# Kernel optimization log

Hardware: AMD Instinct MI355X
Metric: run time of the kernel (lower is better)

## Reference

```python
import jax, jax.numpy as jnp
import numpy as np

HEADS = 8
DIM_HEAD = 64
TOP_K = 1024
KMEANS_ITERS = 4  # the original KMeans class is external; we use Lloyd's algorithm, init = first TOP_K points


def chan_ln(x, g, b):
    # ChanLayerNorm3D: normalize over channel dim (axis=1), biased variance
    m = x.mean(axis=1, keepdims=True)
    v = x.var(axis=1, keepdims=True)
    return g.reshape(1, -1, 1, 1, 1) * (x - m) / (jnp.sqrt(v) + 1e-6) + b.reshape(1, -1, 1, 1, 1)


def kmeans_fit(x, k, iters):
    # x: [N, d] -> centroids [k, d]
    cent0 = x[:k]

    def step(_, cent):
        d2 = (x * x).sum(-1, keepdims=True) - 2.0 * (x @ cent.T) + (cent * cent).sum(-1)
        assign = jnp.argmin(d2, axis=-1)
        sums = jax.ops.segment_sum(x, assign, num_segments=k)
        cnt = jax.ops.segment_sum(jnp.ones((x.shape[0],), x.dtype), assign, num_segments=k)
        new = sums / jnp.maximum(cnt, 1.0)[:, None]
        return jnp.where(cnt[:, None] > 0, new, cent)  # keep old centroid for empty clusters

    return jax.lax.fori_loop(0, iters, step, cent0)


def select_best_idx(q, k, top_k):
    # q: [B, i, d], k: [B, j, d] -> indices [B, top_k] of keys farthest (L1) from their assigned q-centroid
    B, j, d = k.shape
    qf = q.reshape(-1, d)
    kf = k.reshape(-1, d)
    cent = kmeans_fit(qf, top_k, KMEANS_ITERS)
    d2 = (kf * kf).sum(-1, keepdims=True) - 2.0 * (kf @ cent.T) + (cent * cent).sum(-1)
    kc = jnp.argmin(d2, axis=-1)  # predict cluster of each key
    centers = cent[kc].reshape(B, j, d)
    dist = jnp.abs(centers - k).sum(-1)  # [B, j], L1 distance to assigned centroid
    return jnp.argsort(-dist, axis=1)[:, :top_k]


def dpca(query_source, context, w_q, w_kv, w_out, cn_g, cn_b, qn_g, qn_b, on_g, on_b, gamma):
    b, c, D, H, W = query_source.shape
    ctx = chan_ln(context, cn_g, cn_b)
    qs = chan_ln(query_source, qn_g, qn_b)
    # 1x1x1 convs == per-voxel channel matmuls
    kv = jnp.einsum('oc,bcdhw->bodhw', w_kv, ctx)
    k3, v3 = jnp.split(kv, 2, axis=1)
    q3 = jnp.einsum('oc,bcdhw->bodhw', w_q, qs)

    def fold_flat(t, norm):
        bb = t.shape[0]
        t = t.reshape(bb * HEADS, DIM_HEAD, *t.shape[2:])  # fold heads into batch
        if norm:  # F.normalize over channel dim, eps=1e-12
            t = t / jnp.maximum(jnp.linalg.norm(t, axis=1, keepdims=True), 1e-12)
        return t.reshape(bb * HEADS, DIM_HEAD, -1).transpose(0, 2, 1)  # [B, tokens, d]

    q = fold_flat(q3, True)
    k = fold_flat(k3, True)
    v = fold_flat(v3, False)

    idx = select_best_idx(jax.lax.stop_gradient(q), jax.lax.stop_gradient(k), TOP_K)
    k = jnp.take_along_axis(k, idx[:, :, None], axis=1)
    v = jnp.take_along_axis(v, idx[:, :, None], axis=1)

    attn = jax.nn.softmax(jnp.einsum('bid,bjd->bij', q, k), axis=-1)
    out = jnp.einsum('bij,bjd->bid', attn, v)
    out = out.reshape(b, HEADS, D, H, W, DIM_HEAD).transpose(0, 1, 5, 2, 3, 4)
    out = out.reshape(b, HEADS * DIM_HEAD, D, H, W)
    out = jnp.einsum('oc,bcdhw->bodhw', w_out, out)
    out = chan_ln(out, on_g, on_b)
    return gamma * out + query_source


def setup_inputs() -> dict:
    key = jax.random.key(0)
    ks = jax.random.split(key, 6)
    dim, inner, b = 256, HEADS * DIM_HEAD, 2
    query_source = jax.random.normal(ks[0], (b, dim, 16, 16, 16), jnp.float32)
    context = jax.random.normal(ks[1], (b, dim, 8, 16, 16), jnp.float32)
    s_in = 1.0 / np.sqrt(dim)
    return {
        'query_source': query_source,
        'context': context,
        'w_q': jax.random.normal(ks[2], (inner, dim), jnp.float32) * s_in,
        'w_kv': jax.random.normal(ks[3], (2 * inner, dim), jnp.float32) * s_in,
        'w_out': jax.random.normal(ks[4], (dim, inner), jnp.float32) * (1.0 / np.sqrt(inner)),
        'cn_g': jnp.ones((dim,), jnp.float32), 'cn_b': jnp.zeros((dim,), jnp.float32),
        'qn_g': jnp.ones((dim,), jnp.float32), 'qn_b': jnp.zeros((dim,), jnp.float32),
        'on_g': jnp.ones((dim,), jnp.float32), 'on_b': jnp.zeros((dim,), jnp.float32),
        'gamma': jnp.full((1,), 0.5, jnp.float32),  # torch inits to 0 (trivial output); 0.5 makes the test meaningful
    }


def reference(query_source, context, w_q, w_kv, w_out, cn_g, cn_b, qn_g, qn_b, on_g, on_b, gamma):
    return dpca(query_source, context, w_q, w_kv, w_out, cn_g, cn_b, qn_g, qn_b, on_g, on_b, gamma)
```

## Files before the change

### kernel.cpp

```cpp
#include <hip/hip_runtime.h>
#include <math.h>

#define BB 2
#define CDIM 256
#define NQ 4096
#define NK 2048
#define BH 16
#define TOPK 1024
#define NPQ (BH*NQ)
#define NPK (BH*NK)

typedef __attribute__((ext_vector_type(8))) short bfx8;
typedef __attribute__((ext_vector_type(8))) _Float16 hfx8;
typedef __attribute__((ext_vector_type(2))) __fp16 fpx2;
typedef __attribute__((ext_vector_type(4))) float fx4;
typedef __attribute__((ext_vector_type(4))) unsigned short us4;

__device__ inline unsigned short f2bf(float x) {
  unsigned u = __float_as_uint(x);
  return (unsigned short)((u + 0x7fffu + ((u >> 16) & 1u)) >> 16);
}
__device__ inline unsigned short f2h_bits(float x) {
  _Float16 h = (_Float16)x;
  unsigned short u;
  __builtin_memcpy(&u, &h, 2);
  return u;
}
__device__ inline float h_bits2f(unsigned short u) {
  _Float16 h;
  __builtin_memcpy(&h, &u, 2);
  return (float)h;
}

__global__ __launch_bounds__(256) void chan_ln_tsplit_k(
    const float* __restrict__ x, const float* __restrict__ g,
    const float* __restrict__ bta, unsigned short* __restrict__ yh,
    unsigned short* __restrict__ yl, int C, int N) {
  __shared__ float tile[4][64][65];
  __shared__ float p1[4][64], p2[4][64];
  __shared__ float mArr[64], invArr[64];
  int t = threadIdx.x, lane = t & 63, wv = t >> 6;
  int n0 = blockIdx.x * 64, bi = blockIdx.y;
  const float* xb = x + (size_t)bi * C * N + n0 + lane;
  float s = 0.f, s2 = 0.f;
  for (int cl = 0; cl < 64; ++cl) {
    float v = xb[(size_t)(wv * 64 + cl) * N];
    tile[wv][cl][lane] = v;
    s += v;
    s2 += v * v;
  }
  p1[wv][lane] = s;
  p2[wv][lane] = s2;
  __syncthreads();
  if (t < 64) {
    float ts = p1[0][t] + p1[1][t] + p1[2][t] + p1[3][t];
    float ts2 = p2[0][t] + p2[1][t] + p2[2][t] + p2[3][t];
    float m = ts / C;
    float var = ts2 / C - m * m;
    mArr[t] = m;
    invArr[t] = 1.f / (sqrtf(fmaxf(var, 0.f)) + 1e-6f);
  }
  __syncthreads();
  int c = wv * 64 + lane;
  float gc = g[c], bc = bta[c];
  unsigned short* ohb = yh + ((size_t)bi * N + n0) * C + c;
  unsigned short* olb = yl + ((size_t)bi * N + n0) * C + c;
  for (int pl = 0; pl < 64; ++pl) {
    float v = tile[wv][lane][pl];
    float ln = gc * (v - mArr[pl]) * invArr[pl] + bc;
    unsigned short hb = f2h_bits(ln);
    ohb[(size_t)pl * C] = hb;
    olb[(size_t)pl * C] = f2h_bits((ln - h_bits2f(hb)) * 2048.f);
  }
}

__global__ __launch_bounds__(256) void gemm_mfma_k(
    const float* __restrict__ W, const unsigned short* __restrict__ Xh,
    const unsigned short* __restrict__ Xl, float* __restrict__ Y,
    int O, int C, int N) {
  __shared__ __align__(16) unsigned short xlds[2][64][64];
  int t = threadIdx.x, lane = t & 63, wv = t >> 6;
  int lq = lane & 15, lg = lane >> 4;
  int n0 = blockIdx.x * 64, o0 = blockIdx.y * 64 + wv * 16;
  int b = blockIdx.z;
  const unsigned short* xbh = Xh + ((size_t)b * N + n0) * C;
  const unsigned short* xbl = Xl + ((size_t)b * N + n0) * C;
  const float* wr = W + (size_t)(o0 + lq) * C;

  int a = t * 16;
  int srow = a >> 6;
  int schunk = (a >> 4) & 3;
  const unsigned short* gsh = xbh + (size_t)srow * C + schunk * 8;
  const unsigned short* gsl = xbl + (size_t)srow * C + schunk * 8;
  int swz = (srow & 7) << 4;
  int wbh = srow * 128 + ((schunk * 16) ^ swz);
  int wbl = srow * 128 + ((64 + schunk * 16) ^ swz);
  int rswz = (lq & 7) << 4;
  int xh0 = (lg * 16) ^ rswz;
  int xl0 = (64 + lg * 16) ^ rswz;

  fx4 ahi[4], alo[4];
  for (int nt = 0; nt < 4; ++nt) {
    ahi[nt] = (fx4){0.f, 0.f, 0.f, 0.f};
    alo[nt] = (fx4){0.f, 0.f, 0.f, 0.f};
  }

  {
    uint4 h0 = *(const uint4*)(gsh);
    uint4 l0 = *(const uint4*)(gsl);
    *(uint4*)((char*)&xlds[0][0][0] + wbh) = h0;
    *(uint4*)((char*)&xlds[0][0][0] + wbl) = l0;
  }
  float4 w0c = *(const float4*)(wr + lg * 8);
  float4 w1c = *(const float4*)(wr + lg * 8 + 4);

  int nsteps = C / 32;
  for (int s = 0; s < nsteps; ++s) {
    int cur = s & 1;
    __syncthreads();
    uint4 nh, nl;
    float4 nw0, nw1;
    if (s < nsteps - 1) {
      nh = *(const uint4*)(gsh + (s + 1) * 32);
      nl = *(const uint4*)(gsl + (s + 1) * 32);
      nw0 = *(const float4*)(wr + (s + 1) * 32 + lg * 8);
      nw1 = *(const float4*)(wr + (s + 1) * 32 + lg * 8 + 4);
    }
    __builtin_amdgcn_sched_barrier(0);
    float wv8[8] = {w0c.x, w0c.y, w0c.z, w0c.w, w1c.x, w1c.y, w1c.z, w1c.w};
    hfx8 ah, al;
#pragma unroll
    for (int i = 0; i < 8; ++i) {
      _Float16 hh = (_Float16)wv8[i];
      ah[i] = hh;
      al[i] = (_Float16)((wv8[i] - (float)hh) * 2048.f);
    }
    const char* Xb = (const char*)&xlds[cur][0][0];
#pragma unroll
    for (int nt = 0; nt < 4; ++nt) {
      int rb = (nt * 16 + lq) * 128;
      hfx8 bh = *(const hfx8*)(Xb + rb + xh0);
      hfx8 bl = *(const hfx8*)(Xb + rb + xl0);
      ahi[nt] = __builtin_amdgcn_mfma_f32_16x16x32_f16(ah, bh, ahi[nt], 0, 0, 0);
      alo[nt] = __builtin_amdgcn_mfma_f32_16x16x32_f16(al, bh, alo[nt], 0, 0, 0);
      alo[nt] = __builtin_amdgcn_mfma_f32_16x16x32_f16(ah, bl, alo[nt], 0, 0, 0);
    }
    __builtin_amdgcn_sched_barrier(0);
    if (s < nsteps - 1) {
      *(uint4*)((char*)&xlds[cur ^ 1][0][0] + wbh) = nh;
      *(uint4*)((char*)&xlds[cur ^ 1][0][0] + wbl) = nl;
      w0c = nw0;
      w1c = nw1;
    }
  }
  float* yb = Y + ((size_t)b * O + o0) * N + n0;
#pragma unroll
  for (int nt = 0; nt < 4; ++nt)
#pragma unroll
    for (int r = 0; r < 4; ++r)
      yb[(size_t)(lg * 4 + r) * N + nt * 16 + lq] = ahi[nt][r] + alo[nt][r] * (1.f / 2048.f);
}

template <int PATH>
__global__ __launch_bounds__(256) void gemmfold_k(
    const float* __restrict__ W, const unsigned short* __restrict__ Xh,
    const unsigned short* __restrict__ Xl, float* __restrict__ fq,
    unsigned short* __restrict__ sh, unsigned short* __restrict__ sl,
    unsigned short* __restrict__ b16, float* __restrict__ fv,
    int C, int N) {
  __shared__ __align__(16) unsigned short xlds[2][64][64];
  __shared__ float ftile[64][65];
  __shared__ float part[4][64];
  __shared__ float invArr[64];
  int t = threadIdx.x, lane = t & 63, wv = t >> 6;
  int lq = lane & 15, lg = lane >> 4;
  int n0 = blockIdx.x * 64, o0 = blockIdx.y * 64 + wv * 16;
  int b = blockIdx.z;
  bool isV = (PATH == 1) && (blockIdx.y >= 8);
  int h = (PATH == 1) ? (blockIdx.y & 7) : blockIdx.y;
  const unsigned short* xbh = Xh + ((size_t)b * N + n0) * C;
  const unsigned short* xbl = Xl + ((size_t)b * N + n0) * C;
  const float* wr = W + (size_t)(o0 + lq) * C;

  int a = t * 16;
  int srow = a >> 6;
  int schunk = (a >> 4) & 3;
  const unsigned short* gsh = xbh + (size_t)srow * C + schunk * 8;
  const unsigned short* gsl = xbl + (size_t)srow * C + schunk * 8;
  int swz = (srow & 7) << 4;
  int wbh = srow * 128 + ((schunk * 16) ^ swz);
  int wbl = srow * 128 + ((64 + schunk * 16) ^ swz);
  int rswz = (lq & 7) << 4;
  int xh0 = (lg * 16) ^ rswz;
  int xl0 = (64 + lg * 16) ^ rswz;

  fx4 ahi[4], alo[4];
  for (int nt = 0; nt < 4; ++nt) {
    ahi[nt] = (fx4){0.f, 0.f, 0.f, 0.f};
    alo[nt] = (fx4){0.f, 0.f, 0.f, 0.f};
  }

  {
    uint4 h0 = *(const uint4*)(gsh);
    uint4 l0 = *(const uint4*)(gsl);
    *(uint4*)((char*)&xlds[0][0][0] + wbh) = h0;
    *(uint4*)((char*)&xlds[0][0][0] + wbl) = l0;
  }
  float4 w0c = *(const float4*)(wr + lg * 8);
  float4 w1c = *(const float4*)(wr + lg * 8 + 4);

  for (int s = 0; s < 8; ++s) {
    int cur = s & 1;
    __syncthreads();
    uint4 nh, nl;
    float4 nw0, nw1;
    if (s < 7) {
      nh = *(const uint4*)(gsh + (s + 1) * 32);
      nl = *(const uint4*)(gsl + (s + 1) * 32);
      nw0 = *(const float4*)(wr + (s + 1) * 32 + lg * 8);
      nw1 = *(const float4*)(wr + (s + 1) * 32 + lg * 8 + 4);
    }
    __builtin_amdgcn_sched_barrier(0);
    float wv8[8] = {w0c.x, w0c.y, w0c.z, w0c.w, w1c.x, w1c.y, w1c.z, w1c.w};
    hfx8 ah, al;
#pragma unroll
    for (int i = 0; i < 8; ++i) {
      _Float16 hh = (_Float16)wv8[i];
      ah[i] = hh;
      al[i] = (_Float16)((wv8[i] - (float)hh) * 2048.f);
    }
    const char* Xb = (const char*)&xlds[cur][0][0];
#pragma unroll
    for (int nt = 0; nt < 4; ++nt) {
      int rb = (nt * 16 + lq) * 128;
      hfx8 bh = *(const hfx8*)(Xb + rb + xh0);
      hfx8 bl = *(const hfx8*)(Xb + rb + xl0);
      ahi[nt] = __builtin_amdgcn_mfma_f32_16x16x32_f16(ah, bh, ahi[nt], 0, 0, 0);
      alo[nt] = __builtin_amdgcn_mfma_f32_16x16x32_f16(al, bh, alo[nt], 0, 0, 0);
      alo[nt] = __builtin_amdgcn_mfma_f32_16x16x32_f16(ah, bl, alo[nt], 0, 0, 0);
    }
    __builtin_amdgcn_sched_barrier(0);
    if (s < 7) {
      *(uint4*)((char*)&xlds[cur ^ 1][0][0] + wbh) = nh;
      *(uint4*)((char*)&xlds[cur ^ 1][0][0] + wbl) = nl;
      w0c = nw0;
      w1c = nw1;
    }
  }

  float val[4][4];
#pragma unroll
  for (int nt = 0; nt < 4; ++nt)
#pragma unroll
    for (int r = 0; r < 4; ++r)
      val[nt][r] = ahi[nt][r] + alo[nt][r] * (1.f / 2048.f);
  __syncthreads();
  if (!isV) {
#pragma unroll
    for (int nt = 0; nt < 4; ++nt) {
      float ss = val[nt][0] * val[nt][0] + val[nt][1] * val[nt][1] +
                 val[nt][2] * val[nt][2] + val[nt][3] * val[nt][3];
      ss += __shfl_xor(ss, 16);
      ss += __shfl_xor(ss, 32);
      if (lg == 0) part[wv][nt * 16 + lq] = ss;
    }
    __syncthreads();
    if (t < 64) {
      float tot = part[0][t] + part[1][t] + part[2][t] + part[3][t];
      invArr[t] = 1.f / fmaxf(sqrtf(tot), 1e-12f);
    }
    __syncthreads();
#pragma unroll
    for (int nt = 0; nt < 4; ++nt) {
      float iv = invArr[nt * 16 + lq];
#pragma unroll
      for (int r = 0; r < 4; ++r) val[nt][r] *= iv;
    }
    __syncthreads();
  }
#pragma unroll
  for (int nt = 0; nt < 4; ++nt)
#pragma unroll
    for (int r = 0; r < 4; ++r)
      ftile[nt * 16 + lq][wv * 16 + lg * 4 + r] = val[nt][r];
  __syncthreads();
  size_t rowb = (size_t)(b * 8 + h) * N + n0;
  for (int r2 = 0; r2 < 16; ++r2) {
    int n = r2 * 4 + wv;
    float v = ftile[n][lane];
    size_t idx = (rowb + n) * 64 + lane;
    if (PATH == 1 && isV) {
      fv[idx] = v;
    } else {
      fq[idx] = v;
      unsigned short hb = f2h_bits(v);
      sh[idx] = hb;
      sl[idx] = f2h_bits((v - h_bits2f(hb)) * 2048.f);
      if (PATH == 0) b16[idx] = hb;
    }
  }
}

__global__ void centprep_k(const float* __restrict__ cent, float* __restrict__ csq,
                           unsigned short* __restrict__ cb2h, unsigned short* __restrict__ cb2l) {
  int j = blockIdx.x, lane = threadIdx.x;
  float c = cent[j * 64 + lane];
  float s = c * c;
  for (int off = 32; off; off >>= 1) s += __shfl_xor(s, off);
  if (lane == 0) csq[j] = s;
  float m2 = -2.f * c;
  unsigned short h = f2h_bits(m2);
  cb2h[j * 64 + lane] = h;
  cb2l[j * 64 + lane] = f2h_bits((m2 - h_bits2f(h)) * 2048.f);
}

template <int DUO>
__global__ __launch_bounds__(256) void assign_mfma_k(
    const unsigned short* __restrict__ xh, const unsigned short* __restrict__ xl,
    const unsigned short* __restrict__ cb2h, const unsigned short* __restrict__ cb2l,
    const float* __restrict__ csq, int* __restrict__ aout) {
  __shared__ __align__(16) unsigned short clds[4][2][1024];
  int t = threadIdx.x, lane = t & 63, wv = t >> 6;
  int lq = lane & 15, lg = lane >> 4;
  int p0 = blockIdx.x * (DUO ? 128 : 64) + wv * (DUO ? 32 : 16);
  const unsigned short* xbA = xh + (size_t)(p0 + lq) * 64;
  const unsigned short* xlA = xl + (size_t)(p0 + lq) * 64;
  hfx8 ba0 = *(const hfx8*)(xbA + lg * 8);
  hfx8 ba1 = *(const hfx8*)(xbA + 32 + lg * 8);
  hfx8 la0 = *(const hfx8*)(xlA + lg * 8);
  hfx8 la1 = *(const hfx8*)(xlA + 32 + lg * 8);
  hfx8 bb0, bb1, lb0, lb1;
  if (DUO) {
    const unsigned short* xbB = xh + (size_t)(p0 + 16 + lq) * 64;
    const unsigned short* xlB = xl + (size_t)(p0 + 16 + lq) * 64;
    bb0 = *(const hfx8*)(xbB + lg * 8);
    bb1 = *(const hfx8*)(xbB + 32 + lg * 8);
    lb0 = *(const hfx8*)(xlB + lg * 8);
    lb1 = *(const hfx8*)(xlB + 32 + lg * 8);
  }

  int part = t >> 7;
  int abyte = (t & 127) * 16;
  int wbyte = abyte ^ (((abyte >> 7) & 7) << 4);
  const unsigned short* gsrc = (part ? cb2l : cb2h) + (abyte >> 1);
  int rowoff = lq * 128;
  int x0 = (lg * 16) ^ ((lq & 7) << 4);
  int x1 = (64 + lg * 16) ^ ((lq & 7) << 4);

  float bestA = 3.4e38f, bestB = 3.4e38f;
  int jA = 0, jB = 0;

  fx4 pchi0A, pclo0A, pchi1A, pclo1A;
  fx4 pchi0B, pclo0B, pchi1B, pclo1B;

  {
    uint4 r0 = *(const uint4*)(gsrc);
    uint4 r1 = *(const uint4*)(gsrc + 1024);
    *(uint4*)((char*)&clds[0][part][0] + wbyte) = r0;
    *(uint4*)((char*)&clds[1][part][0] + wbyte) = r1;
  }

#define COMPARE_PREV(SBASE)                                                    \
  {                                                                            \
    _Pragma("unroll")                                                          \
    for (int u = 0; u < 2; ++u) {                                              \
      int st_ = (SBASE) + u;                                                   \
      fx4 chi_ = u ? pchi1A : pchi0A;                                          \
      fx4 clo_ = u ? pclo1A : pclo0A;                                          \
      _Pragma("unroll")                                                        \
      for (int r_ = 0; r_ < 4; ++r_) {                                         \
        int j_ = st_ * 16 + lg * 4 + r_;                                       \
        float d2_ = chi_[r_] + clo_[r_] * (1.f / 2048.f);                      \
        if (d2_ < bestA) { bestA = d2_; jA = j_; }                             \
      }                                                                        \
      if (DUO) {                                                               \
        fx4 chiB_ = u ? pchi1B : pchi0B;                                       \
        fx4 cloB_ = u ? pclo1B : pclo0B;                                       \
        _Pragma("unroll")                                                      \
        for (int r_ = 0; r_ < 4; ++r_) {                                       \
          int j_ = st_ * 16 + lg * 4 + r_;                                     \
          float d2_ = chiB_[r_] + cloB_[r_] * (1.f / 2048.f);                  \
          if (d2_ < bestB) { bestB = d2_; jB = j_; }                           \
        }                                                                      \
      }                                                                        \
    }                                                                          \
  }

  for (int s = 0; s < 64; s += 2) {
    __syncthreads();
    uint4 rn0, rn1;
    if (s < 62) {
      rn0 = *(const uint4*)(gsrc + (size_t)(s + 2) * 1024);
      rn1 = *(const uint4*)(gsrc + (size_t)(s + 3) * 1024);
    }
    __builtin_amdgcn_sched_barrier(0);
    fx4 cchi0A, cclo0A, cchi1A, cclo1A;
    fx4 cchi0B, cclo0B, cchi1B, cclo1B;
#pragma unroll
    for (int u = 0; u < 2; ++u) {
      int st = s + u;
      const char* ph = (const char*)&clds[st & 3][0][0];
      const char* pl = (const char*)&clds[st & 3][1][0];
      hfx8 ah0 = *(const hfx8*)(ph + rowoff + x0);
      hfx8 ah1 = *(const hfx8*)(ph + rowoff + x1);
      hfx8 al0 = *(const hfx8*)(pl + rowoff + x0);
      hfx8 al1 = *(const hfx8*)(pl + rowoff + x1);
      fx4 cq = *(const fx4*)(csq + st * 16 + lg * 4);
      {
        fx4 chi = cq;
        chi = __builtin_amdgcn_mfma_f32_16x16x32_f16(ah0, ba0, chi, 0, 0, 0);
        chi = __builtin_amdgcn_mfma_f32_16x16x32_f16(ah1, ba1, chi, 0, 0, 0);
        fx4 clo = (fx4){0.f, 0.f, 0.f, 0.f};
        clo = __builtin_amdgcn_mfma_f32_16x16x32_f16(ah0, la0, clo, 0, 0, 0);
        clo = __builtin_amdgcn_mfma_f32_16x16x32_f16(ah1, la1, clo, 0, 0, 0);
        clo = __builtin_amdgcn_mfma_f32_16x16x32_f16(al0, ba0, clo, 0, 0, 0);
        clo = __builtin_amdgcn_mfma_f32_16x16x32_f16(al1, ba1, clo, 0, 0, 0);
        if (u == 0) { cchi0A = chi; cclo0A = clo; } else { cchi1A = chi; cclo1A = clo; }
      }
      if (DUO) {
        fx4 chi = cq;
        chi = __builtin_amdgcn_mfma_f32_16x16x32_f16(ah0, bb0, chi, 0, 0, 0);
        chi = __builtin_amdgcn_mfma_f32_16x16x32_f16(ah1, bb1, chi, 0, 0, 0);
        fx4 clo = (fx4){0.f, 0.f, 0.f, 0.f};
        clo = __builtin_amdgcn_mfma_f32_16x16x32_f16(ah0, lb0, clo, 0, 0, 0);
        clo = __builtin_amdgcn_mfma_f32_16x16x32_f16(ah1, lb1, clo, 0, 0, 0);
        clo = __builtin_amdgcn_mfma_f32_16x16x32_f16(al0, lb0 * (_Float16)0 + bb0, clo, 0, 0, 0);
        clo = __builtin_amdgcn_mfma_f32_16x16x32_f16(al1, bb1, clo, 0, 0, 0);
        if (u == 0) { cchi0B = chi; cclo0B = clo; } else { cchi1B = chi; cclo1B = clo; }
      }
    }
    if (s > 0) COMPARE_PREV(s - 2);
    pchi0A = cchi0A; pclo0A = cclo0A; pchi1A = cchi1A; pclo1A = cclo1A;
    if (DUO) { pchi0B = cchi0B; pclo0B = cclo0B; pchi1B = cchi1B; pclo1B = cclo1B; }
    __builtin_amdgcn_sched_barrier(0);
    if (s < 62) {
      *(uint4*)((char*)&clds[(s + 2) & 3][part][0] + wbyte) = rn0;
      *(uint4*)((char*)&clds[(s + 3) & 3][part][0] + wbyte) = rn1;
    }
  }
  COMPARE_PREV(62);
#undef COMPARE_PREV

  {
    float o = __shfl_xor(bestA, 16);
    int oj = __shfl_xor(jA, 16);
    if (o < bestA || (o == bestA && oj < jA)) { bestA = o; jA = oj; }
    o = __shfl_xor(bestA, 32);
    oj = __shfl_xor(jA, 32);
    if (o < bestA || (o == bestA && oj < jA)) { bestA = o; jA = oj; }
  }
  if (DUO) {
    float o = __shfl_xor(bestB, 16);
    int oj = __shfl_xor(jB, 16);
    if (o < bestB || (o == bestB && oj < jB)) { bestB = o; jB = oj; }
    o = __shfl_xor(bestB, 32);
    oj = __shfl_xor(jB, 32);
    if (o < bestB || (o == bestB && oj < jB)) { bestB = o; jB = oj; }
  }
  if (lg == 0) {
    aout[p0 + lq] = jA;
    if (DUO) aout[p0 + 16 + lq] = jB;
  }
}

__global__ void dist_k(const float* __restrict__ x, const float* __restrict__ cent,
                       const int* __restrict__ asg, float* __restrict__ dout) {
  int t = threadIdx.x, lane = t & 63, wv = t >> 6;
  int p = blockIdx.x * 4 + wv;
  int a = asg[p];
  float v = fabsf(cent[(size_t)a * 64 + lane] - x[(size_t)p * 64 + lane]);
  for (int off = 32; off; off >>= 1) v += __shfl_xor(v, off);
  if (lane == 0) dout[p] = v;
}

__global__ void segsum_k(const float* __restrict__ x, const int* __restrict__ asg,
                         float* __restrict__ sums, float* __restrict__ cnt) {
  int t = threadIdx.x, lane = t & 63, wv = t >> 6;
  int p = blockIdx.x * 4 + wv;
  int a = asg[p];
  float v = x[(size_t)p * 64 + lane];
  atomicAdd(&sums[a * 64 + lane], v);
  if (lane == 0) atomicAdd(&cnt[a], 1.0f);
}

__global__ __launch_bounds__(256) void centup_prep_k(
    float* __restrict__ cent, float* __restrict__ sums, float* __restrict__ cnt,
    float* __restrict__ csq, unsigned short* __restrict__ cb2h,
    unsigned short* __restrict__ cb2l) {
  int i = blockIdx.x * 256 + threadIdx.x;
  int j = i >> 6, lane = threadIdx.x & 63;
  float c = cnt[j];
  float oldc = cent[i];
  float newc = (c > 0.f) ? sums[i] / fmaxf(c, 1.f) : oldc;
  cent[i] = newc;
  float s = newc * newc;
  for (int off = 32; off; off >>= 1) s += __shfl_xor(s, off);
  if (lane == 0) csq[j] = s;
  float m2 = -2.f * newc;
  unsigned short h = f2h_bits(m2);
  cb2h[i] = h;
  cb2l[i] = f2h_bits((m2 - h_bits2f(h)) * 2048.f);
  sums[i] = 0.f;
  if (lane == 0) cnt[j] = 0.f;
}

__global__ __launch_bounds__(1024) void topk_k(const float* __restrict__ dist,
                                               int* __restrict__ sel) {
  __shared__ unsigned long long keys[2048];
  int bh = blockIdx.x, t = threadIdx.x;
  for (int i = t; i < 2048; i += 1024) {
    float d = dist[bh * 2048 + i];
    unsigned int db = __float_as_uint(d);
    keys[i] = ((unsigned long long)db << 32) | (unsigned int)(2047 - i);
  }
  __syncthreads();
  for (int k = 2; k <= 2048; k <<= 1) {
    for (int j = k >> 1; j > 0; j >>= 1) {
      for (int i = t; i < 2048; i += 1024) {
        int ixj = i ^ j;
        if (ixj > i) {
          unsigned long long a = keys[i], b = keys[ixj];
          bool up = ((i & k) == 0);
          bool sw = up ? (a < b) : (a > b);
          if (sw) { keys[i] = b; keys[ixj] = a; }
        }
      }
      __syncthreads();
    }
  }
  if (t < 1024) sel[bh * 1024 + t] = 2047 - (int)(keys[t] & 0xffffffffu);
}

__global__ void gatherb_k(const float* __restrict__ kbuf, const float* __restrict__ vbuf,
                          const int* __restrict__ sel, unsigned short* __restrict__ kh,
                          unsigned short* __restrict__ vT) {
  __shared__ unsigned short tile[64][66];
  int t = threadIdx.x, lane = t & 63, wv = t >> 6;
  int bh = blockIdx.y, i0 = blockIdx.x * 64;
  for (int r = 0; r < 16; ++r) {
    int i = r * 4 + wv;
    int src = sel[bh * 1024 + i0 + i];
    float kvv = kbuf[((size_t)bh * 2048 + src) * 64 + lane];
    kh[((size_t)bh * 1024 + i0 + i) * 64 + lane] = f2h_bits(kvv);
    float vv = vbuf[((size_t)bh * 2048 + src) * 64 + lane];
    tile[i][lane] = f2h_bits(vv);
  }
  __syncthreads();
  for (int r = 0; r < 16; ++r) {
    int d = r * 4 + wv;
    vT[((size_t)bh * 64 + d) * 1024 + i0 + lane] = tile[lane][d];
  }
}

__global__ __launch_bounds__(256) void attn_mfma_k(
    const unsigned short* __restrict__ qh, const unsigned short* __restrict__ kh,
    const unsigned short* __restrict__ vT,
    unsigned short* __restrict__ oh, unsigned short* __restrict__ ol) {
  __shared__ __align__(16) unsigned short kvlds[2][2][4096];
  __shared__ __align__(16) unsigned short plds[4][16][72];
  int t = threadIdx.x, lane = t & 63, wv = t >> 6;
  int lq = lane & 15, lg = lane >> 4;
  int id = blockIdx.x;
  int bh = (id & 7) * 2 + ((id >> 3) & 1);
  int q0 = (id >> 4) * 64 + wv * 16;
  const unsigned short* qbase = qh + ((size_t)bh * 4096 + q0 + lq) * 64;
  hfx8 qf0 = *(const hfx8*)(qbase + lg * 8);
  hfx8 qf1 = *(const hfx8*)(qbase + 32 + lg * 8);
  fx4 acc[4];
  for (int nt = 0; nt < 4; ++nt) acc[nt] = (fx4){0.f, 0.f, 0.f, 0.f};
  float lsum = 0.f;
  const unsigned short* kbase = kh + (size_t)bh * 1024 * 64;
  const unsigned short* vbase = vT + (size_t)bh * 64 * 1024;

  int srow = t >> 2;
  int scolb = (t & 3) * 32;
  const char* gK = (const char*)kbase + (size_t)srow * 128 + scolb;
  const char* gV = (const char*)vbase + (size_t)srow * 2048 + scolb;
  int sw_w = (srow & 7) << 4;
  int wb0 = srow * 128 + (scolb ^ sw_w);
  int wb1 = srow * 128 + ((scolb + 16) ^ sw_w);

  {
    uint4 k0 = *(const uint4*)(gK);
    uint4 k1 = *(const uint4*)(gK + 16);
    uint4 v0 = *(const uint4*)(gV);
    uint4 v1 = *(const uint4*)(gV + 16);
    *(uint4*)((char*)&kvlds[0][0][0] + wb0) = k0;
    *(uint4*)((char*)&kvlds[0][0][0] + wb1) = k1;
    *(uint4*)((char*)&kvlds[0][1][0] + wb0) = v0;
    *(uint4*)((char*)&kvlds[0][1][0] + wb1) = v1;
  }

  int swr = (lq & 7) << 4;
  int rc0 = (lg * 16) ^ swr;
  int rc1 = (64 + lg * 16) ^ swr;

  for (int s = 0; s < 16; ++s) {
    int cur = s & 1;
    __syncthreads();
    uint4 nk0, nk1, nv0, nv1;
    if (s < 15) {
      const char* gKn = gK + (size_t)(s + 1) * 8192;
      const char* gVn = gV + (size_t)(s + 1) * 128;
      nk0 = *(const uint4*)(gKn);
      nk1 = *(const uint4*)(gKn + 16);
      nv0 = *(const uint4*)(gVn);
      nv1 = *(const uint4*)(gVn + 16);
    }
    __builtin_amdgcn_sched_barrier(0);
    const char* Kb = (const char*)&kvlds[cur][0][0];
    const char* Vb = (const char*)&kvlds[cur][1][0];
    fx4 sS[4];
#pragma unroll
    for (int mt = 0; mt < 4; ++mt) {
      int rowb = (mt * 16 + lq) * 128;
      hfx8 a0 = *(const hfx8*)(Kb + rowb + rc0);
      hfx8 a1 = *(const hfx8*)(Kb + rowb + rc1);
      fx4 c = (fx4){0.f, 0.f, 0.f, 0.f};
      c = __builtin_amdgcn_mfma_f32_16x16x32_f16(a0, qf0, c, 0, 0, 0);
      c = __builtin_amdgcn_mfma_f32_16x16x32_f16(a1, qf1, c, 0, 0, 0);
      sS[mt] = c;
    }
#pragma unroll
    for (int mt = 0; mt < 4; ++mt) {
      float p0 = __expf(sS[mt].x), p1 = __expf(sS[mt].y);
      float p2 = __expf(sS[mt].z), p3 = __expf(sS[mt].w);
      lsum += (p0 + p1) + (p2 + p3);
      fpx2 c01 = __builtin_amdgcn_cvt_pkrtz(p0, p1);
      fpx2 c23 = __builtin_amdgcn_cvt_pkrtz(p2, p3);
      unsigned u01, u23;
      __builtin_memcpy(&u01, &c01, 4);
      __builtin_memcpy(&u23, &c23, 4);
      uint2 pk = {u01, u23};
      *(uint2*)&plds[wv][lq][mt * 16 + lg * 4] = pk;
    }
    hfx8 pa0 = *(const hfx8*)&plds[wv][lq][lg * 8];
    hfx8 pa1 = *(const hfx8*)&plds[wv][lq][32 + lg * 8];
#pragma unroll
    for (int nt = 0; nt < 4; ++nt) {
      int rowb = (nt * 16 + lq) * 128;
      hfx8 b0 = *(const hfx8*)(Vb + rowb + rc0);
      hfx8 b1 = *(const hfx8*)(Vb + rowb + rc1);
      acc[nt] = __builtin_amdgcn_mfma_f32_16x16x32_f16(pa0, b0, acc[nt], 0, 0, 0);
      acc[nt] = __builtin_amdgcn_mfma_f32_16x16x32_f16(pa1, b1, acc[nt], 0, 0, 0);
    }
    __builtin_amdgcn_sched_barrier(0);
    if (s < 15) {
      char* dK = (char*)&kvlds[cur ^ 1][0][0];
      char* dV = (char*)&kvlds[cur ^ 1][1][0];
      *(uint4*)(dK + wb0) = nk0;
      *(uint4*)(dK + wb1) = nk1;
      *(uint4*)(dV + wb0) = nv0;
      *(uint4*)(dV + wb1) = nv1;
    }
  }
  lsum += __shfl_xor(lsum, 16);
  lsum += __shfl_xor(lsum, 32);
  int bi = bh >> 3, hd = bh & 7;
  for (int r = 0; r < 4; ++r) {
    float inv = 1.f / __shfl(lsum, lg * 4 + r);
    size_t rowb = ((size_t)bi * 4096 + q0 + lg * 4 + r) * 512 + hd * 64;
    for (int nt = 0; nt < 4; ++nt) {
      float val = acc[nt][r] * inv;
      unsigned short hb = f2h_bits(val);
      oh[rowb + nt * 16 + lq] = hb;
      ol[rowb + nt * 16 + lq] = f2h_bits((val - h_bits2f(hb)) * 2048.f);
    }
  }
}

__global__ __launch_bounds__(256) void final_k(
    const float* __restrict__ y, const float* __restrict__ g,
    const float* __restrict__ bta, const float* __restrict__ gamma,
    const float* __restrict__ qs, float* __restrict__ out) {
  __shared__ float p1[4][64], p2[4][64];
  __shared__ float mArr[64], invArr[64];
  int t = threadIdx.x, lane = t & 63, wv = t >> 6;
  int n0 = blockIdx.x * 64, bi = blockIdx.y;
  const float* yb = y + (size_t)bi * CDIM * NQ + n0 + lane;
  float s = 0.f, s2 = 0.f;
  for (int cl = 0; cl < 64; ++cl) {
    float v = yb[(size_t)(wv * 64 + cl) * NQ];
    s += v;
    s2 += v * v;
  }
  p1[wv][lane] = s;
  p2[wv][lane] = s2;
  __syncthreads();
  if (t < 64) {
    float ts = p1[0][t] + p1[1][t] + p1[2][t] + p1[3][t];
    float ts2 = p2[0][t] + p2[1][t] + p2[2][t] + p2[3][t];
    float m = ts / CDIM;
    float var = ts2 / CDIM - m * m;
    mArr[t] = m;
    invArr[t] = 1.f / (sqrtf(fmaxf(var, 0.f)) + 1e-6f);
  }
  __syncthreads();
  float gm = gamma[0];
  float m = mArr[lane], inv = invArr[lane];
  const float* qb = qs + (size_t)bi * CDIM * NQ + n0 + lane;
  float* ob = out + (size_t)bi * CDIM * NQ + n0 + lane;
  for (int cl = 0; cl < 64; ++cl) {
    int c = wv * 64 + cl;
    float v = yb[(size_t)c * NQ];
    float ln = g[c] * (v - m) * inv + bta[c];
    ob[(size_t)c * NQ] = gm * ln + qb[(size_t)c * NQ];
  }
}

extern "C" void kernel_launch(void* const* d_in, const int* in_sizes, int n_in,
                              void* d_out, int out_size, void* d_ws, size_t ws_size,
                              hipStream_t stream) {
  const float* qsrc = (const float*)d_in[0];
  const float* ctx = (const float*)d_in[1];
  const float* w_q = (const float*)d_in[2];
  const float* w_kv = (const float*)d_in[3];
  const float* w_out = (const float*)d_in[4];
  const float* cn_g = (const float*)d_in[5];
  const float* cn_b = (const float*)d_in[6];
  const float* qn_g = (const float*)d_in[7];
  const float* qn_b = (const float*)d_in[8];
  const float* on_g = (const float*)d_in[9];
  const float* on_b = (const float*)d_in[10];
  const float* gamma = (const float*)d_in[11];

  if (ws_size < (size_t)22267904 * 4) return;
  float* ws = (float*)d_ws;
  float* r_ctx = ws;
  float* r_kv = r_ctx + 1048576;
  float* r_qs = r_kv + 4194304;
  float* r_q3 = r_qs + 2097152;
  float* qbuf = r_q3 + 4194304;
  float* kbuf = qbuf + 4194304;
  float* vbuf = kbuf + 2097152;
  float* cent = vbuf + 2097152;
  float* csq = cent + 65536;
  float* sums = csq + 1024;
  float* cnt = sums + 65536;
  int* asg = (int*)(cnt + 1024);
  float* dist = (float*)(asg + 65536);
  int* sel = (int*)(dist + 32768);
  float* kgreg = (float*)(sel + 16384);

  unsigned short* ctxth = (unsigned short*)r_ctx;
  unsigned short* ctxtl = ctxth + (size_t)BB * NK * CDIM;
  unsigned short* qsth = (unsigned short*)r_qs;
  unsigned short* qstl = qsth + (size_t)BB * NQ * CDIM;
  unsigned short* qh = (unsigned short*)kgreg;
  unsigned short* kh = (unsigned short*)r_ctx;
  unsigned short* vT = kh + 1048576;
  unsigned short* qbh = (unsigned short*)r_q3;
  unsigned short* qbl = qbh + (size_t)NPQ * 64;
  unsigned short* kbh = (unsigned short*)r_kv;
  unsigned short* kbl = kbh + (size_t)NPK * 64;
  unsigned short* cb2h = (unsigned short*)r_qs;
  unsigned short* cb2l = cb2h + 65536;
  unsigned short* attnth = (unsigned short*)r_kv;
  unsigned short* attntl = attnth + (size_t)BB * NQ * 512;
  float* ybuf = r_qs;

  chan_ln_tsplit_k<<<dim3(NK / 64, BB), 256, 0, stream>>>(ctx, cn_g, cn_b, ctxth, ctxtl, CDIM, NK);
  chan_ln_tsplit_k<<<dim3(NQ / 64, BB), 256, 0, stream>>>(qsrc, qn_g, qn_b, qsth, qstl, CDIM, NQ);
  gemmfold_k<1><<<dim3(NK / 64, 16, BB), 256, 0, stream>>>(
      w_kv, ctxth, ctxtl, kbuf, kbh, kbl, nullptr, vbuf, CDIM, NK);
  gemmfold_k<0><<<dim3(NQ / 64, 8, BB), 256, 0, stream>>>(
      w_q, qsth, qstl, qbuf, qbh, qbl, qh, nullptr, CDIM, NQ);
  hipMemcpyAsync(cent, qbuf, 65536 * sizeof(float), hipMemcpyDeviceToDevice, stream);
  centprep_k<<<1024, 64, 0, stream>>>(cent, csq, cb2h, cb2l);
  hipMemsetAsync(sums, 0, (65536 + 1024) * sizeof(float), stream);
  for (int it = 0; it < 4; ++it) {
    assign_mfma_k<1><<<NPQ / 128, 256, 0, stream>>>(qbh, qbl, cb2h, cb2l, csq, asg);
    segsum_k<<<NPQ / 4, 256, 0, stream>>>(qbuf, asg, sums, cnt);
    centup_prep_k<<<65536 / 256, 256, 0, stream>>>(cent, sums, cnt, csq, cb2h, cb2l);
  }
  assign_mfma_k<0><<<NPK / 64, 256, 0, stream>>>(kbh, kbl, cb2h, cb2l, csq, asg);
  dist_k<<<NPK / 4, 256, 0, stream>>>(kbuf, cent, asg, dist);
  topk_k<<<BH, 1024, 0, stream>>>(dist, sel);
  gatherb_k<<<dim3(TOPK / 64, BH), 256, 0, stream>>>(kbuf, vbuf, sel, kh, vT);
  attn_mfma_k<<<1024, 256, 0, stream>>>(qh, kh, vT, attnth, attntl);
  gemm_mfma_k<<<dim3(NQ / 64, 256 / 64, BB), 256, 0, stream>>>(w_out, attnth, attntl, ybuf, 256, 512, NQ);
  final_k<<<dim3(NQ / 64, BB), 256, 0, stream>>>(ybuf, on_g, on_b, gamma, qsrc, (float*)d_out);
}
```

Baseline: 482.9 us.

## Load V fragments directly from global in attention; use single-tile assign for kmeans

The attention kernel no longer stages V through LDS. Each wave loads its V MFMA operands straight from global memory into registers at the start of every key tile, which halves LDS traffic and shared-memory footprint and may raise occupancy. The cost is that V loads are now issued per wave without the shared double buffer, so the same data is fetched repeatedly and load latency sits on the critical path. Separately, the kmeans assign launch switches from the two-tile (DUO) variant to the single-tile one with twice as many blocks, and a redundant multiply-by-zero expression in the DUO path is simplified.

```diff
diff --git a/kernel.cpp b/kernel.cpp
--- a/kernel.cpp
+++ b/kernel.cpp
@@ -424,7 +424,7 @@
         fx4 clo = (fx4){0.f, 0.f, 0.f, 0.f};
         clo = __builtin_amdgcn_mfma_f32_16x16x32_f16(ah0, lb0, clo, 0, 0, 0);
         clo = __builtin_amdgcn_mfma_f32_16x16x32_f16(ah1, lb1, clo, 0, 0, 0);
-        clo = __builtin_amdgcn_mfma_f32_16x16x32_f16(al0, lb0 * (_Float16)0 + bb0, clo, 0, 0, 0);
+        clo = __builtin_amdgcn_mfma_f32_16x16x32_f16(al0, bb0, clo, 0, 0, 0);
         clo = __builtin_amdgcn_mfma_f32_16x16x32_f16(al1, bb1, clo, 0, 0, 0);
         if (u == 0) { cchi0B = chi; cclo0B = clo; } else { cchi1B = chi; cclo1B = clo; }
       }
@@ -556,7 +556,7 @@
     const unsigned short* __restrict__ qh, const unsigned short* __restrict__ kh,
     const unsigned short* __restrict__ vT,
     unsigned short* __restrict__ oh, unsigned short* __restrict__ ol) {
-  __shared__ __align__(16) unsigned short kvlds[2][2][4096];
+  __shared__ __align__(16) unsigned short klds[2][4096];
   __shared__ __align__(16) unsigned short plds[4][16][72];
   int t = threadIdx.x, lane = t & 63, wv = t >> 6;
   int lq = lane & 15, lg = lane >> 4;
@@ -575,7 +575,6 @@
   int srow = t >> 2;
   int scolb = (t & 3) * 32;
   const char* gK = (const char*)kbase + (size_t)srow * 128 + scolb;
-  const char* gV = (const char*)vbase + (size_t)srow * 2048 + scolb;
   int sw_w = (srow & 7) << 4;
   int wb0 = srow * 128 + (scolb ^ sw_w);
   int wb1 = srow * 128 + ((scolb + 16) ^ sw_w);
@@ -583,12 +582,8 @@
   {
     uint4 k0 = *(const uint4*)(gK);
     uint4 k1 = *(const uint4*)(gK + 16);
-    uint4 v0 = *(const uint4*)(gV);
-    uint4 v1 = *(const uint4*)(gV + 16);
-    *(uint4*)((char*)&kvlds[0][0][0] + wb0) = k0;
-    *(uint4*)((char*)&kvlds[0][0][0] + wb1) = k1;
-    *(uint4*)((char*)&kvlds[0][1][0] + wb0) = v0;
-    *(uint4*)((char*)&kvlds[0][1][0] + wb1) = v1;
+    *(uint4*)((char*)&klds[0][0] + wb0) = k0;
+    *(uint4*)((char*)&klds[0][0] + wb1) = k1;
   }
 
   int swr = (lq & 7) << 4;
@@ -597,19 +592,23 @@
 
   for (int s = 0; s < 16; ++s) {
     int cur = s & 1;
+    int kt0 = s * 64;
     __syncthreads();
-    uint4 nk0, nk1, nv0, nv1;
+    hfx8 vb0[4], vb1[4];
+#pragma unroll
+    for (int nt = 0; nt < 4; ++nt) {
+      const unsigned short* vr = vbase + (size_t)(nt * 16 + lq) * 1024 + kt0 + lg * 8;
+      vb0[nt] = *(const hfx8*)(vr);
+      vb1[nt] = *(const hfx8*)(vr + 32);
+    }
+    uint4 nk0, nk1;
     if (s < 15) {
       const char* gKn = gK + (size_t)(s + 1) * 8192;
-      const char* gVn = gV + (size_t)(s + 1) * 128;
       nk0 = *(const uint4*)(gKn);
       nk1 = *(const uint4*)(gKn + 16);
-      nv0 = *(const uint4*)(gVn);
-      nv1 = *(const uint4*)(gVn + 16);
     }
     __builtin_amdgcn_sched_barrier(0);
-    const char* Kb = (const char*)&kvlds[cur][0][0];
-    const char* Vb = (const char*)&kvlds[cur][1][0];
+    const char* Kb = (const char*)&klds[cur][0];
     fx4 sS[4];
 #pragma unroll
     for (int mt = 0; mt < 4; ++mt) {
@@ -638,20 +637,14 @@
     hfx8 pa1 = *(const hfx8*)&plds[wv][lq][32 + lg * 8];
 #pragma unroll
     for (int nt = 0; nt < 4; ++nt) {
-      int rowb = (nt * 16 + lq) * 128;
-      hfx8 b0 = *(const hfx8*)(Vb + rowb + rc0);
-      hfx8 b1 = *(const hfx8*)(Vb + rowb + rc1);
-      acc[nt] = __builtin_amdgcn_mfma_f32_16x16x32_f16(pa0, b0, acc[nt], 0, 0, 0);
-      acc[nt] = __builtin_amdgcn_mfma_f32_16x16x32_f16(pa1, b1, acc[nt], 0, 0, 0);
+      acc[nt] = __builtin_amdgcn_mfma_f32_16x16x32_f16(pa0, vb0[nt], acc[nt], 0, 0, 0);
+      acc[nt] = __builtin_amdgcn_mfma_f32_16x16x32_f16(pa1, vb1[nt], acc[nt], 0, 0, 0);
     }
     __builtin_amdgcn_sched_barrier(0);
     if (s < 15) {
-      char* dK = (char*)&kvlds[cur ^ 1][0][0];
-      char* dV = (char*)&kvlds[cur ^ 1][1][0];
+      char* dK = (char*)&klds[cur ^ 1][0];
       *(uint4*)(dK + wb0) = nk0;
       *(uint4*)(dK + wb1) = nk1;
-      *(uint4*)(dV + wb0) = nv0;
-      *(uint4*)(dV + wb1) = nv1;
     }
   }
   lsum += __shfl_xor(lsum, 16);
@@ -769,7 +762,7 @@
   centprep_k<<<1024, 64, 0, stream>>>(cent, csq, cb2h, cb2l);
   hipMemsetAsync(sums, 0, (65536 + 1024) * sizeof(float), stream);
   for (int it = 0; it < 4; ++it) {
-    assign_mfma_k<1><<<NPQ / 128, 256, 0, stream>>>(qbh, qbl, cb2h, cb2l, csq, asg);
+    assign_mfma_k<0><<<NPQ / 64, 256, 0, stream>>>(qbh, qbl, cb2h, cb2l, csq, asg);
     segsum_k<<<NPQ / 4, 256, 0, stream>>>(qbuf, asg, sums, cnt);
     centup_prep_k<<<65536 / 256, 256, 0, stream>>>(cent, sums, cnt, csq, cb2h, cb2l);
   }
```

After: 525.2 us. 8.8% more time.
